# Performance work log

Measured on AMD Instinct MI355X. Metric: run time of the kernel, lower is better.

## Reference

```python
import jax, jax.numpy as jnp
import numpy as np
import math

D_MODEL = 1024
N_HEADS = 16
D_K = D_MODEL // N_HEADS


def setup_inputs() -> dict:
    key = jax.random.key(0)
    ks = jax.random.split(key, 5)
    std = math.sqrt(2.0 / (D_MODEL + D_MODEL))
    x = jax.random.normal(ks[0], (2, 2048, D_MODEL), dtype=jnp.float32)
    W_q = jax.random.normal(ks[1], (D_MODEL, D_MODEL), dtype=jnp.float32) * std
    W_k = jax.random.normal(ks[2], (D_MODEL, D_MODEL), dtype=jnp.float32) * std
    W_v = jax.random.normal(ks[3], (D_MODEL, D_MODEL), dtype=jnp.float32) * std
    W_o = jax.random.normal(ks[4], (D_MODEL, D_MODEL), dtype=jnp.float32) * std
    return {"x": x, "W_q": W_q, "W_k": W_k, "W_v": W_v, "W_o": W_o}


def reference(x, W_q, W_k, W_v, W_o):
    B, S, D = x.shape
    H, dk = N_HEADS, D_K
    # projections: (B,S,D) @ (D,D)
    def split_heads(t):  # (B,S,D) -> (B,H,S,dk)
        return t.reshape(B, S, H, dk).transpose(0, 2, 1, 3)
    Q = split_heads(x @ W_q)
    K = split_heads(x @ W_k)
    V = split_heads(x @ W_v)
    scale = 1.0 / math.sqrt(dk)
    scores = jnp.einsum("bhqd,bhkd->bhqk", Q, K) * scale  # (B,H,S,S)
    attn = jax.nn.softmax(scores, axis=-1)
    out = jnp.einsum("bhqk,bhkd->bhqd", attn, V)  # (B,H,S,dk)
    concat = out.transpose(0, 2, 1, 3).reshape(B, S, D)
    return concat @ W_o
```

## Files before the change

### kernel.cpp

```cpp
#include <hip/hip_runtime.h>
#include <hip/hip_bf16.h>
#include <math.h>

#define DMODEL 1024
#define NHEADS 16
#define DKH    64
#define BATCH  2
#define SEQ    2048
#define MROWS  (BATCH * SEQ)
#define LOG2E  1.4426950408889634f

typedef __bf16 bf16_t;
typedef bf16_t bf16x8 __attribute__((ext_vector_type(8)));
typedef bf16_t bf16x4 __attribute__((ext_vector_type(4)));
typedef float  floatx4 __attribute__((ext_vector_type(4)));

__device__ __forceinline__ void glds16(const bf16_t* g, bf16_t* l) {
    __builtin_amdgcn_global_load_lds((__attribute__((address_space(1))) unsigned*)(g),
                                     (__attribute__((address_space(3))) unsigned*)(l),
                                     16, 0, 0);
}

__global__ void cast_x_kernel(const float* __restrict__ x, bf16_t* __restrict__ xb) {
    int i = (blockIdx.x * 256 + threadIdx.x) * 4;
    float4 v = *(const float4*)(x + i);
    bf16_t o0 = (bf16_t)v.x, o1 = (bf16_t)v.y, o2 = (bf16_t)v.z, o3 = (bf16_t)v.w;
    bf16_t o[4] = {o0, o1, o2, o3};
    *(uint2*)(xb + i) = *(uint2*)o;
}

__global__ void transpose4_kernel(const float* __restrict__ W0, const float* __restrict__ W1,
                                  const float* __restrict__ W2, const float* __restrict__ W3,
                                  bf16_t* __restrict__ Wt) {
    __shared__ float t[32][33];
    const float* W = (blockIdx.z == 0) ? W0 : (blockIdx.z == 1) ? W1 : (blockIdx.z == 2) ? W2 : W3;
    bf16_t* dst = Wt + (size_t)blockIdx.z * DMODEL * DMODEL;
    int bx = blockIdx.x, by = blockIdx.y;
    int tx = threadIdx.x, ty = threadIdx.y;
#pragma unroll
    for (int i = 0; i < 32; i += 8)
        t[ty + i][tx] = W[(size_t)(by * 32 + ty + i) * DMODEL + bx * 32 + tx];
    __syncthreads();
#pragma unroll
    for (int i = 0; i < 32; i += 8)
        dst[(size_t)(bx * 32 + ty + i) * DMODEL + by * 32 + tx] = (bf16_t)t[tx][ty + i];
}

template<int MODE>
__global__ __launch_bounds__(256) void gemm128_kernel(const bf16_t* __restrict__ A,
                                                      const bf16_t* __restrict__ Bt,
                                                      void* __restrict__ outp) {
    __shared__ bf16_t As[128 * 64];
    __shared__ bf16_t Bs[128 * 64];
    int tid = threadIdx.x;
    int w = tid >> 6, l = tid & 63, g = l >> 4, lm = l & 15;
    int wr = w >> 1, wc = w & 1;
    int m0 = blockIdx.y * 128, n0 = blockIdx.x * 128;
    int r8 = l >> 3, s8 = l & 7, cw = s8 ^ r8;

    floatx4 acc[4][4];
#pragma unroll
    for (int i = 0; i < 4; ++i)
#pragma unroll
        for (int j = 0; j < 4; ++j) { floatx4 z = {0.f, 0.f, 0.f, 0.f}; acc[i][j] = z; }

    const bf16_t* Ag = A  + (size_t)(m0 + w * 32 + r8) * DMODEL + cw * 8;
    const bf16_t* Bg = Bt + (size_t)(n0 + w * 32 + r8) * DMODEL + cw * 8;

    for (int k0 = 0; k0 < DMODEL; k0 += 64) {
        __syncthreads();
#pragma unroll
        for (int j = 0; j < 4; ++j) {
            glds16(Ag + (size_t)j * 8 * DMODEL + k0, &As[(w * 32 + j * 8) * 64]);
            glds16(Bg + (size_t)j * 8 * DMODEL + k0, &Bs[(w * 32 + j * 8) * 64]);
        }
        __syncthreads();
#pragma unroll
        for (int kk = 0; kk < 2; ++kk) {
            bf16x8 af[4], bfr[4];
            int c = kk * 4 + g;
            int sw = (c ^ (lm & 7)) * 8;
#pragma unroll
            for (int i = 0; i < 4; ++i) {
                af[i]  = *(const bf16x8*)&As[(wr * 64 + i * 16 + lm) * 64 + sw];
                bfr[i] = *(const bf16x8*)&Bs[(wc * 64 + i * 16 + lm) * 64 + sw];
            }
#pragma unroll
            for (int i = 0; i < 4; ++i)
#pragma unroll
                for (int j = 0; j < 4; ++j)
                    acc[i][j] = __builtin_amdgcn_mfma_f32_16x16x32_bf16(af[i], bfr[j], acc[i][j], 0, 0, 0);
        }
    }

    const size_t NX = (size_t)MROWS * DMODEL;
#pragma unroll
    for (int i = 0; i < 4; ++i) {
#pragma unroll
        for (int j = 0; j < 4; ++j) {
            int nc = n0 + wc * 64 + j * 16 + lm;
            int mb = m0 + wr * 64 + i * 16 + g * 4;
            if (MODE == 0) {
                int mat = n0 >> 10;
                int col = nc & 1023;
                int b = mb >> 11, hh = col >> 6, d = col & 63;
                bf16_t* base = (bf16_t*)outp;
                if (mat == 2) {
                    int s = mb & 2047;
                    bf16x4 pk = {(bf16_t)acc[i][j][0], (bf16_t)acc[i][j][1],
                                 (bf16_t)acc[i][j][2], (bf16_t)acc[i][j][3]};
                    *(bf16x4*)&(base + 2 * NX)[(((size_t)(b * NHEADS + hh)) * DKH + d) * SEQ + s] = pk;
                } else {
#pragma unroll
                    for (int r = 0; r < 4; ++r) {
                        float v = acc[i][j][r];
                        int s = (mb + r) & 2047;
                        if (mat == 0)
                            base[(((size_t)(b * NHEADS + hh)) * SEQ + s) * DKH + d] = (bf16_t)(v * (0.125f * LOG2E));
                        else
                            (base + NX)[(((size_t)(b * NHEADS + hh)) * SEQ + s) * DKH + d] = (bf16_t)v;
                    }
                }
            } else {
#pragma unroll
                for (int r = 0; r < 4; ++r)
                    ((float*)outp)[(size_t)(mb + r) * DMODEL + nc] = acc[i][j][r];
            }
        }
    }
}

__device__ __forceinline__ int swz(int row, int c4) {
    return row * 64 + ((c4 ^ (row & 14)) << 2);
}

__global__ __launch_bounds__(256, 1) void attn_kernel(const bf16_t* __restrict__ Q,
                                                      const bf16_t* __restrict__ K,
                                                      const bf16_t* __restrict__ Vt,
                                                      bf16_t* __restrict__ Cc) {
    __shared__ bf16_t Ks[2][64 * 64];
    __shared__ bf16_t Vs[2][64 * 64];
    __shared__ bf16_t Ps[4][64 * 64];

    int tid = threadIdx.x;
    int w = tid >> 6, l = tid & 63, g = l >> 4, lm = l & 15;
    int bh = blockIdx.x, b = bh >> 4, h = bh & 15;
    int q0 = blockIdx.y * 256;
    int qw = q0 + w * 64;
    int xsw = lm & 14;

    const bf16_t* Qh  = Q  + (size_t)bh * SEQ * DKH;
    const bf16_t* Kh  = K  + (size_t)bh * SEQ * DKH;
    const bf16_t* Vth = Vt + (size_t)bh * DKH * SEQ;

    bf16x8 qf[4][2];
#pragma unroll
    for (int nt = 0; nt < 4; ++nt)
#pragma unroll
        for (int kk = 0; kk < 2; ++kk)
            qf[nt][kk] = *(const bf16x8*)(Qh + (size_t)(qw + nt * 16 + lm) * DKH + kk * 32 + g * 8);

    int r0 = tid >> 3, r1 = (tid + 256) >> 3;
    int cc4 = (tid & 7) * 2;
    int d0 = swz(r0, cc4), d1 = swz(r1, cc4);
    int gc = (tid & 7) * 8;

    bf16x8 kreg0, kreg1, vreg0, vreg1;
    kreg0 = *(const bf16x8*)(Kh + (size_t)r0 * DKH + gc);
    kreg1 = *(const bf16x8*)(Kh + (size_t)r1 * DKH + gc);
    vreg0 = *(const bf16x8*)(Vth + (size_t)r0 * SEQ + gc);
    vreg1 = *(const bf16x8*)(Vth + (size_t)r1 * SEQ + gc);
    *(bf16x8*)&Ks[0][d0] = kreg0;  *(bf16x8*)&Ks[0][d1] = kreg1;
    *(bf16x8*)&Vs[0][d0] = vreg0;  *(bf16x8*)&Vs[0][d1] = vreg1;
    kreg0 = *(const bf16x8*)(Kh + (size_t)(64 + r0) * DKH + gc);
    kreg1 = *(const bf16x8*)(Kh + (size_t)(64 + r1) * DKH + gc);
    vreg0 = *(const bf16x8*)(Vth + (size_t)r0 * SEQ + 64 + gc);
    vreg1 = *(const bf16x8*)(Vth + (size_t)r1 * SEQ + 64 + gc);

    floatx4 oacc[4][4];
#pragma unroll
    for (int dt = 0; dt < 4; ++dt)
#pragma unroll
        for (int nt = 0; nt < 4; ++nt) { floatx4 z = {0.f, 0.f, 0.f, 0.f}; oacc[dt][nt] = z; }
    float lsum[4] = {0.f, 0.f, 0.f, 0.f};

    for (int kt = 0; kt < SEQ / 64; ++kt) {
        int cb = kt & 1, nb = cb ^ 1;
        __syncthreads();
        if (kt + 1 < SEQ / 64) {
            *(bf16x8*)&Ks[nb][d0] = kreg0;  *(bf16x8*)&Ks[nb][d1] = kreg1;
            *(bf16x8*)&Vs[nb][d0] = vreg0;  *(bf16x8*)&Vs[nb][d1] = vreg1;
        }
        if (kt + 2 < SEQ / 64) {
            int t2 = (kt + 2) * 64;
            kreg0 = *(const bf16x8*)(Kh + (size_t)(t2 + r0) * DKH + gc);
            kreg1 = *(const bf16x8*)(Kh + (size_t)(t2 + r1) * DKH + gc);
            vreg0 = *(const bf16x8*)(Vth + (size_t)r0 * SEQ + t2 + gc);
            vreg1 = *(const bf16x8*)(Vth + (size_t)r1 * SEQ + t2 + gc);
        }

        floatx4 sacc[4][4];
#pragma unroll
        for (int mt = 0; mt < 4; ++mt)
#pragma unroll
            for (int nt = 0; nt < 4; ++nt) { floatx4 z = {0.f, 0.f, 0.f, 0.f}; sacc[mt][nt] = z; }
#pragma unroll
        for (int kk = 0; kk < 2; ++kk) {
            bf16x8 ak[4];
#pragma unroll
            for (int mt = 0; mt < 4; ++mt)
                ak[mt] = *(const bf16x8*)&Ks[cb][(mt * 16 + lm) * 64 + (((kk * 8 + g * 2) ^ xsw) << 2)];
#pragma unroll
            for (int mt = 0; mt < 4; ++mt)
#pragma unroll
                for (int nt = 0; nt < 4; ++nt)
                    sacc[mt][nt] = __builtin_amdgcn_mfma_f32_16x16x32_bf16(ak[mt], qf[nt][kk], sacc[mt][nt], 0, 0, 0);
        }

#pragma unroll
        for (int mt = 0; mt < 4; ++mt)
#pragma unroll
            for (int nt = 0; nt < 4; ++nt) {
                float p0 = __builtin_amdgcn_exp2f(sacc[mt][nt][0]);
                float p1 = __builtin_amdgcn_exp2f(sacc[mt][nt][1]);
                float p2 = __builtin_amdgcn_exp2f(sacc[mt][nt][2]);
                float p3 = __builtin_amdgcn_exp2f(sacc[mt][nt][3]);
                lsum[nt] += (p0 + p1) + (p2 + p3);
                bf16x4 pk = {(bf16_t)p0, (bf16_t)p1, (bf16_t)p2, (bf16_t)p3};
                *(bf16x4*)&Ps[w][(nt * 16 + lm) * 64 + (((mt * 4 + g) ^ xsw) << 2)] = pk;
            }

#pragma unroll
        for (int kk = 0; kk < 2; ++kk) {
            bf16x8 av[4], bp[4];
#pragma unroll
            for (int dt = 0; dt < 4; ++dt)
                av[dt] = *(const bf16x8*)&Vs[cb][(dt * 16 + lm) * 64 + (((kk * 8 + g * 2) ^ xsw) << 2)];
#pragma unroll
            for (int nt = 0; nt < 4; ++nt)
                bp[nt] = *(const bf16x8*)&Ps[w][(nt * 16 + lm) * 64 + (((kk * 8 + g * 2) ^ xsw) << 2)];
#pragma unroll
            for (int dt = 0; dt < 4; ++dt)
#pragma unroll
                for (int nt = 0; nt < 4; ++nt)
                    oacc[dt][nt] = __builtin_amdgcn_mfma_f32_16x16x32_bf16(av[dt], bp[nt], oacc[dt][nt], 0, 0, 0);
        }
    }

    float linv[4];
#pragma unroll
    for (int nt = 0; nt < 4; ++nt) {
        float s = lsum[nt];
        s += __shfl_xor(s, 16, 64);
        s += __shfl_xor(s, 32, 64);
        linv[nt] = 1.0f / s;
    }

#pragma unroll
    for (int dt = 0; dt < 4; ++dt)
#pragma unroll
        for (int nt = 0; nt < 4; ++nt) {
            bf16x4 pk = {(bf16_t)(oacc[dt][nt][0] * linv[nt]), (bf16_t)(oacc[dt][nt][1] * linv[nt]),
                         (bf16_t)(oacc[dt][nt][2] * linv[nt]), (bf16_t)(oacc[dt][nt][3] * linv[nt])};
            int q = qw + nt * 16 + lm;
            int d = h * DKH + dt * 16 + g * 4;
            *(bf16x4*)&Cc[((size_t)(b * SEQ + q)) * DMODEL + d] = pk;
        }
}

extern "C" void kernel_launch(void* const* d_in, const int* in_sizes, int n_in,
                              void* d_out, int out_size, void* d_ws, size_t ws_size,
                              hipStream_t stream) {
    const float* x  = (const float*)d_in[0];
    const float* Wq = (const float*)d_in[1];
    const float* Wk = (const float*)d_in[2];
    const float* Wv = (const float*)d_in[3];
    const float* Wo = (const float*)d_in[4];

    const size_t NX = (size_t)MROWS * DMODEL;
    const size_t NW = (size_t)DMODEL * DMODEL;
    bf16_t* ws  = (bf16_t*)d_ws;
    bf16_t* xb  = ws;
    bf16_t* Wt  = xb + NX;
    bf16_t* Wto = Wt + 3 * NW;
    bf16_t* Qb  = Wt + 4 * NW;
    bf16_t* Kb  = Qb + NX;
    bf16_t* Vtb = Kb + NX;
    bf16_t* Cc  = Vtb + NX;

    cast_x_kernel<<<NX / 1024, 256, 0, stream>>>(x, xb);
    transpose4_kernel<<<dim3(32, 32, 4), dim3(32, 8), 0, stream>>>(Wq, Wk, Wv, Wo, Wt);

    gemm128_kernel<0><<<dim3(3 * DMODEL / 128, MROWS / 128), 256, 0, stream>>>(xb, Wt, Qb);

    attn_kernel<<<dim3(BATCH * NHEADS, SEQ / 256), 256, 0, stream>>>(Qb, Kb, Vtb, Cc);

    gemm128_kernel<3><<<dim3(DMODEL / 128, MROWS / 128), 256, 0, stream>>>(Cc, Wto, (float*)d_out);
}
```

Baseline: 200.8 us.

## Split attention KV range across warps, load K/V directly from global

The attention kernel now gives each block 128 queries, with warp pairs splitting the key sequence in half (split-K). The two partial outputs are merged through shared memory at the end. K and V fragments are read straight from global memory into registers, replacing the shared-memory double buffer and per-tile barriers. The row sum is computed with an MFMA against a ones vector instead of scalar adds, and the grid doubles to raise occupancy (launch bounds 2). The risks are uncoalesced, redundant global K/V loads and no software prefetch.

```diff
diff --git a/kernel.cpp b/kernel.cpp
--- a/kernel.cpp
+++ b/kernel.cpp
@@ -130,26 +130,21 @@
     }
 }
 
-__device__ __forceinline__ int swz(int row, int c4) {
-    return row * 64 + ((c4 ^ (row & 14)) << 2);
-}
-
-__global__ __launch_bounds__(256, 1) void attn_kernel(const bf16_t* __restrict__ Q,
+__global__ __launch_bounds__(256, 2) void attn_kernel(const bf16_t* __restrict__ Q,
                                                       const bf16_t* __restrict__ K,
                                                       const bf16_t* __restrict__ Vt,
                                                       bf16_t* __restrict__ Cc) {
-    __shared__ bf16_t Ks[2][64 * 64];
-    __shared__ bf16_t Vs[2][64 * 64];
     __shared__ bf16_t Ps[4][64 * 64];
+    __shared__ float  Ms[2][64 * 36];
 
     int tid = threadIdx.x;
     int w = tid >> 6, l = tid & 63, g = l >> 4, lm = l & 15;
+    int qw = w & 1, ks = w >> 1;
     int bh = blockIdx.x, b = bh >> 4, h = bh & 15;
-    int q0 = blockIdx.y * 256;
-    int qw = q0 + w * 64;
+    int q0 = blockIdx.y * 128 + qw * 64;
     int xsw = lm & 14;
 
-    const bf16_t* Qh  = Q  + (size_t)bh * SEQ * DKH;
+    const bf16_t* Qh  = Q  + ((size_t)bh * SEQ + q0) * DKH;
     const bf16_t* Kh  = K  + (size_t)bh * SEQ * DKH;
     const bf16_t* Vth = Vt + (size_t)bh * DKH * SEQ;
 
@@ -158,46 +153,31 @@
     for (int nt = 0; nt < 4; ++nt)
 #pragma unroll
         for (int kk = 0; kk < 2; ++kk)
-            qf[nt][kk] = *(const bf16x8*)(Qh + (size_t)(qw + nt * 16 + lm) * DKH + kk * 32 + g * 8);
-
-    int r0 = tid >> 3, r1 = (tid + 256) >> 3;
-    int cc4 = (tid & 7) * 2;
-    int d0 = swz(r0, cc4), d1 = swz(r1, cc4);
-    int gc = (tid & 7) * 8;
-
-    bf16x8 kreg0, kreg1, vreg0, vreg1;
-    kreg0 = *(const bf16x8*)(Kh + (size_t)r0 * DKH + gc);
-    kreg1 = *(const bf16x8*)(Kh + (size_t)r1 * DKH + gc);
-    vreg0 = *(const bf16x8*)(Vth + (size_t)r0 * SEQ + gc);
-    vreg1 = *(const bf16x8*)(Vth + (size_t)r1 * SEQ + gc);
-    *(bf16x8*)&Ks[0][d0] = kreg0;  *(bf16x8*)&Ks[0][d1] = kreg1;
-    *(bf16x8*)&Vs[0][d0] = vreg0;  *(bf16x8*)&Vs[0][d1] = vreg1;
-    kreg0 = *(const bf16x8*)(Kh + (size_t)(64 + r0) * DKH + gc);
-    kreg1 = *(const bf16x8*)(Kh + (size_t)(64 + r1) * DKH + gc);
-    vreg0 = *(const bf16x8*)(Vth + (size_t)r0 * SEQ + 64 + gc);
-    vreg1 = *(const bf16x8*)(Vth + (size_t)r1 * SEQ + 64 + gc);
+            qf[nt][kk] = *(const bf16x8*)(Qh + (size_t)(nt * 16 + lm) * DKH + kk * 32 + g * 8);
+
+    bf16x8 onesf;
+#pragma unroll
+    for (int j = 0; j < 8; ++j) onesf[j] = (bf16_t)1.0f;
 
     floatx4 oacc[4][4];
 #pragma unroll
     for (int dt = 0; dt < 4; ++dt)
 #pragma unroll
         for (int nt = 0; nt < 4; ++nt) { floatx4 z = {0.f, 0.f, 0.f, 0.f}; oacc[dt][nt] = z; }
-    float lsum[4] = {0.f, 0.f, 0.f, 0.f};
-
-    for (int kt = 0; kt < SEQ / 64; ++kt) {
-        int cb = kt & 1, nb = cb ^ 1;
-        __syncthreads();
-        if (kt + 1 < SEQ / 64) {
-            *(bf16x8*)&Ks[nb][d0] = kreg0;  *(bf16x8*)&Ks[nb][d1] = kreg1;
-            *(bf16x8*)&Vs[nb][d0] = vreg0;  *(bf16x8*)&Vs[nb][d1] = vreg1;
-        }
-        if (kt + 2 < SEQ / 64) {
-            int t2 = (kt + 2) * 64;
-            kreg0 = *(const bf16x8*)(Kh + (size_t)(t2 + r0) * DKH + gc);
-            kreg1 = *(const bf16x8*)(Kh + (size_t)(t2 + r1) * DKH + gc);
-            vreg0 = *(const bf16x8*)(Vth + (size_t)r0 * SEQ + t2 + gc);
-            vreg1 = *(const bf16x8*)(Vth + (size_t)r1 * SEQ + t2 + gc);
-        }
+    floatx4 lacc[4];
+#pragma unroll
+    for (int nt = 0; nt < 4; ++nt) { floatx4 z = {0.f, 0.f, 0.f, 0.f}; lacc[nt] = z; }
+
+    for (int kt = ks * 16; kt < ks * 16 + 16; ++kt) {
+        const bf16_t* Kt  = Kh  + (size_t)kt * 64 * DKH;
+        const bf16_t* Vtt = Vth + kt * 64;
+
+        bf16x8 kf[4][2];
+#pragma unroll
+        for (int mt = 0; mt < 4; ++mt)
+#pragma unroll
+            for (int kk = 0; kk < 2; ++kk)
+                kf[mt][kk] = *(const bf16x8*)(Kt + (size_t)(mt * 16 + lm) * DKH + kk * 32 + g * 8);
 
         floatx4 sacc[4][4];
 #pragma unroll
@@ -205,67 +185,88 @@
 #pragma unroll
             for (int nt = 0; nt < 4; ++nt) { floatx4 z = {0.f, 0.f, 0.f, 0.f}; sacc[mt][nt] = z; }
 #pragma unroll
+        for (int kk = 0; kk < 2; ++kk)
+#pragma unroll
+            for (int mt = 0; mt < 4; ++mt)
+#pragma unroll
+                for (int nt = 0; nt < 4; ++nt)
+                    sacc[mt][nt] = __builtin_amdgcn_mfma_f32_16x16x32_bf16(kf[mt][kk], qf[nt][kk], sacc[mt][nt], 0, 0, 0);
+
+        bf16x8 vf[4][2];
+#pragma unroll
+        for (int dt = 0; dt < 4; ++dt)
+#pragma unroll
+            for (int kk = 0; kk < 2; ++kk)
+                vf[dt][kk] = *(const bf16x8*)(Vtt + (size_t)(dt * 16 + lm) * SEQ + kk * 32 + g * 8);
+
+#pragma unroll
+        for (int mt = 0; mt < 4; ++mt)
+#pragma unroll
+            for (int nt = 0; nt < 4; ++nt) {
+                bf16x4 pk = {(bf16_t)__builtin_amdgcn_exp2f(sacc[mt][nt][0]),
+                             (bf16_t)__builtin_amdgcn_exp2f(sacc[mt][nt][1]),
+                             (bf16_t)__builtin_amdgcn_exp2f(sacc[mt][nt][2]),
+                             (bf16_t)__builtin_amdgcn_exp2f(sacc[mt][nt][3])};
+                *(bf16x4*)&Ps[w][(nt * 16 + lm) * 64 + (((mt * 4 + g) ^ xsw) << 2)] = pk;
+            }
+
+#pragma unroll
         for (int kk = 0; kk < 2; ++kk) {
-            bf16x8 ak[4];
-#pragma unroll
-            for (int mt = 0; mt < 4; ++mt)
-                ak[mt] = *(const bf16x8*)&Ks[cb][(mt * 16 + lm) * 64 + (((kk * 8 + g * 2) ^ xsw) << 2)];
-#pragma unroll
-            for (int mt = 0; mt < 4; ++mt)
-#pragma unroll
-                for (int nt = 0; nt < 4; ++nt)
-                    sacc[mt][nt] = __builtin_amdgcn_mfma_f32_16x16x32_bf16(ak[mt], qf[nt][kk], sacc[mt][nt], 0, 0, 0);
-        }
-
-#pragma unroll
-        for (int mt = 0; mt < 4; ++mt)
-#pragma unroll
-            for (int nt = 0; nt < 4; ++nt) {
-                float p0 = __builtin_amdgcn_exp2f(sacc[mt][nt][0]);
-                float p1 = __builtin_amdgcn_exp2f(sacc[mt][nt][1]);
-                float p2 = __builtin_amdgcn_exp2f(sacc[mt][nt][2]);
-                float p3 = __builtin_amdgcn_exp2f(sacc[mt][nt][3]);
-                lsum[nt] += (p0 + p1) + (p2 + p3);
-                bf16x4 pk = {(bf16_t)p0, (bf16_t)p1, (bf16_t)p2, (bf16_t)p3};
-                *(bf16x4*)&Ps[w][(nt * 16 + lm) * 64 + (((mt * 4 + g) ^ xsw) << 2)] = pk;
-            }
-
-#pragma unroll
-        for (int kk = 0; kk < 2; ++kk) {
-            bf16x8 av[4], bp[4];
-#pragma unroll
-            for (int dt = 0; dt < 4; ++dt)
-                av[dt] = *(const bf16x8*)&Vs[cb][(dt * 16 + lm) * 64 + (((kk * 8 + g * 2) ^ xsw) << 2)];
+            bf16x8 bp[4];
 #pragma unroll
             for (int nt = 0; nt < 4; ++nt)
                 bp[nt] = *(const bf16x8*)&Ps[w][(nt * 16 + lm) * 64 + (((kk * 8 + g * 2) ^ xsw) << 2)];
 #pragma unroll
+            for (int nt = 0; nt < 4; ++nt)
+                lacc[nt] = __builtin_amdgcn_mfma_f32_16x16x32_bf16(onesf, bp[nt], lacc[nt], 0, 0, 0);
+#pragma unroll
             for (int dt = 0; dt < 4; ++dt)
 #pragma unroll
                 for (int nt = 0; nt < 4; ++nt)
-                    oacc[dt][nt] = __builtin_amdgcn_mfma_f32_16x16x32_bf16(av[dt], bp[nt], oacc[dt][nt], 0, 0, 0);
+                    oacc[dt][nt] = __builtin_amdgcn_mfma_f32_16x16x32_bf16(vf[dt][kk], bp[nt], oacc[dt][nt], 0, 0, 0);
         }
     }
 
     float linv[4];
 #pragma unroll
-    for (int nt = 0; nt < 4; ++nt) {
-        float s = lsum[nt];
-        s += __shfl_xor(s, 16, 64);
-        s += __shfl_xor(s, 32, 64);
-        linv[nt] = 1.0f / s;
+    for (int pass = 0; pass < 2; ++pass) {
+        __syncthreads();
+        if (ks == 1) {
+#pragma unroll
+            for (int dh = 0; dh < 2; ++dh) {
+                int dt = pass * 2 + dh;
+#pragma unroll
+                for (int nt = 0; nt < 4; ++nt)
+                    *(floatx4*)&Ms[qw][(nt * 16 + lm) * 36 + dh * 16 + g * 4] = oacc[dt][nt];
+            }
+            if (pass == 0 && g == 0)
+#pragma unroll
+                for (int nt = 0; nt < 4; ++nt)
+                    Ms[qw][(nt * 16 + lm) * 36 + 32] = lacc[nt][0];
+        }
+        __syncthreads();
+        if (ks == 0) {
+            if (pass == 0)
+#pragma unroll
+                for (int nt = 0; nt < 4; ++nt)
+                    linv[nt] = 1.0f / (lacc[nt][0] + Ms[qw][(nt * 16 + lm) * 36 + 32]);
+#pragma unroll
+            for (int dh = 0; dh < 2; ++dh) {
+                int dt = pass * 2 + dh;
+#pragma unroll
+                for (int nt = 0; nt < 4; ++nt) {
+                    floatx4 part = *(const floatx4*)&Ms[qw][(nt * 16 + lm) * 36 + dh * 16 + g * 4];
+                    bf16x4 pk = {(bf16_t)((oacc[dt][nt][0] + part[0]) * linv[nt]),
+                                 (bf16_t)((oacc[dt][nt][1] + part[1]) * linv[nt]),
+                                 (bf16_t)((oacc[dt][nt][2] + part[2]) * linv[nt]),
+                                 (bf16_t)((oacc[dt][nt][3] + part[3]) * linv[nt])};
+                    int q = q0 + nt * 16 + lm;
+                    int d = h * DKH + dt * 16 + g * 4;
+                    *(bf16x4*)&Cc[((size_t)(b * SEQ + q)) * DMODEL + d] = pk;
+                }
+            }
+        }
     }
-
-#pragma unroll
-    for (int dt = 0; dt < 4; ++dt)
-#pragma unroll
-        for (int nt = 0; nt < 4; ++nt) {
-            bf16x4 pk = {(bf16_t)(oacc[dt][nt][0] * linv[nt]), (bf16_t)(oacc[dt][nt][1] * linv[nt]),
-                         (bf16_t)(oacc[dt][nt][2] * linv[nt]), (bf16_t)(oacc[dt][nt][3] * linv[nt])};
-            int q = qw + nt * 16 + lm;
-            int d = h * DKH + dt * 16 + g * 4;
-            *(bf16x4*)&Cc[((size_t)(b * SEQ + q)) * DMODEL + d] = pk;
-        }
 }
 
 extern "C" void kernel_launch(void* const* d_in, const int* in_sizes, int n_in,
@@ -293,7 +294,7 @@
 
     gemm128_kernel<0><<<dim3(3 * DMODEL / 128, MROWS / 128), 256, 0, stream>>>(xb, Wt, Qb);
 
-    attn_kernel<<<dim3(BATCH * NHEADS, SEQ / 256), 256, 0, stream>>>(Qb, Kb, Vtb, Cc);
+    attn_kernel<<<dim3(BATCH * NHEADS, SEQ / 128), 256, 0, stream>>>(Qb, Kb, Vtb, Cc);
 
     gemm128_kernel<3><<<dim3(DMODEL / 128, MROWS / 128), 256, 0, stream>>>(Cc, Wto, (float*)d_out);
 }
```

New measurement: 207.1 us. +3.1%, slower.
